# Kernel tuning notes

Measured on AMD Instinct MI355X. Metric: run time of the kernel, lower is better.

## Reference

```python
import jax, jax.numpy as jnp
import numpy as np

EPS = 1.0  # Shapelet eps
STRIDE = 1


def _shapelet(x, w, pcm):
    """x: (b,c,t), w: (n,c,l), pcm: (c,m). Returns ((b, n*c) probs, (b, n*c) dists)."""
    n, c, l = w.shape
    t = x.shape[-1]
    m = (t - l) // STRIDE + 1
    # unfold: gather overlapping windows -> (b, c, m, l)
    idx = jnp.arange(m)[:, None] * STRIDE + jnp.arange(l)[None, :]
    win = x[:, :, idx]                                   # (b, c, m, l)
    xw = jnp.transpose(win, (0, 2, 1, 3))[:, :, None]    # (b, m, 1, c, l)
    d = jnp.mean(jnp.abs(xw - w), axis=-1)               # (b, m, n, c)
    d = d * pcm.T[None, :, None, :]                      # penalty (1, m, 1, c)
    p = jnp.exp(-jnp.square(EPS * d))                    # (b, m, n, c)
    hard = jax.nn.one_hot(jnp.argmax(p, axis=1), m, axis=1, dtype=p.dtype)  # (b,m,n,c)
    soft = jax.nn.softmax(p, axis=1)
    onehot_max = hard + soft - jax.lax.stop_gradient(soft)  # straight-through
    max_p = jnp.sum(onehot_max * p, axis=1)              # (b, n, c)
    d_min = jnp.min(d, axis=1)                           # (b, n, c)
    b = x.shape[0]
    return max_p.reshape(b, -1), d_min.reshape(b, -1)


def _diversity(w):
    """w: (n,c,l) -> scalar. torch PairwiseDistance(p=2, eps=1e-6) adds eps to diff."""
    sh = jnp.transpose(w, (1, 0, 2))                     # (c, n, l)
    diff = sh[:, None, :, :] - sh[:, :, None, :] + 1e-6
    dist = jnp.sqrt(jnp.sum(jnp.square(diff), axis=-1))  # (c, n, n)
    nsh = sh.shape[1]
    mask = 1.0 - jnp.eye(nsh, dtype=w.dtype)
    return jnp.mean(jnp.exp(-dist) * mask[None])


def setup_inputs() -> dict:
    key = jax.random.key(0)
    ks = jax.random.split(key, 6)
    b, c, t, ncls = 32, 8, 512, 10
    sls = [52, 103, 154, 256]
    ms = [t - l + 1 for l in sls]
    inp = {"x": jax.random.normal(ks[0], (b, c, t), dtype=jnp.float32)}
    for i, (l, m) in enumerate(zip(sls, ms)):
        inp[f"w{i}"] = jax.random.normal(ks[1 + i], (5, c, l), dtype=jnp.float32)
        inp[f"pcm{i}"] = jnp.ones((c, m), dtype=jnp.float32)
    inp["W_out"] = jax.random.normal(ks[5], (ncls, 160), dtype=jnp.float32) * 0.05
    return inp


def reference(x, w0, w1, w2, w3, pcm0, pcm1, pcm2, pcm3, W_out):
    # instance norm over time (torch std is unbiased, ddof=1)
    mu = jnp.mean(x, axis=-1, keepdims=True)
    sd = jnp.std(x, axis=-1, keepdims=True, ddof=1)
    xn = (x - mu) / (sd + 1e-8)

    ws = (w0, w1, w2, w3)
    pcms = (pcm0, pcm1, pcm2, pcm3)
    probs, dists = [], []
    for w, pcm in zip(ws, pcms):
        p, d = _shapelet(xn, w, pcm)
        probs.append(p)
        dists.append(d)
    shapelet_probs = jnp.concatenate(probs, axis=-1)   # (b, 160)
    shapelet_dists = jnp.concatenate(dists, axis=-1)   # (b, 160)

    # dropout is identity in eval mode
    out = shapelet_probs @ W_out.T                     # (b, num_classes)

    loss_reg = jnp.mean(jnp.abs(W_out))
    loss_div = sum(_diversity(w) for w in ws)
    loss = (0.1 * loss_reg + 0.1 * loss_div).reshape(1)
    return out, shapelet_dists, shapelet_probs, loss
```

## Files before the change

### kernel.cpp

```cpp
#include <hip/hip_runtime.h>
#include <math.h>

#define B 32
#define C 8
#define T 512
#define NSH 5
#define NCLS 10
#define NFEAT 160

#define OUT_OFF    0
#define DIST_OFF   (B * NCLS)
#define PROB_OFF   (DIST_OFF + B * NFEAT)
#define LOSS_OFF   (PROB_OFF + B * NFEAT)


template<int L, int M, int GOFF>
__device__ __forceinline__ void shapelet_task(
    const float* __restrict__ x,
    const float* __restrict__ wrow,
    const float* __restrict__ pmrow,
    float* __restrict__ out, int bc, int n)
{
    const int lane = threadIdx.x & 63;
    const int b = bc >> 3, c = bc & 7;
    const float* xrow = x + bc * T;

    const float4 u0 = *(const float4*)(xrow + lane * 4);
    const float4 u1 = *(const float4*)(xrow + 256 + lane * 4);
    float s = u0.x + u0.y + u0.z + u0.w + u1.x + u1.y + u1.z + u1.w;
    #pragma unroll
    for (int off = 32; off; off >>= 1) s += __shfl_down(s, off);
    const float mu = __shfl(s, 0) * (1.0f / T);
    float sq = (u0.x-mu)*(u0.x-mu) + (u0.y-mu)*(u0.y-mu) + (u0.z-mu)*(u0.z-mu) + (u0.w-mu)*(u0.w-mu)
             + (u1.x-mu)*(u1.x-mu) + (u1.y-mu)*(u1.y-mu) + (u1.z-mu)*(u1.z-mu) + (u1.w-mu)*(u1.w-mu);
    #pragma unroll
    for (int off = 32; off; off >>= 1) sq += __shfl_down(sq, off);
    const float var = __shfl(sq, 0) * (1.0f / (T - 1));
    const float ns = 1.0f / (sqrtf(var) + 1e-8f);
    const float nb = -mu * ns;

    const int sbase = lane * 8;
    const int sb = (sbase < M) ? sbase : 0;

    float4 a  = *(const float4*)(xrow + sb);
    float4 bb = *(const float4*)(xrow + sb + 4);
    float4 cc = *(const float4*)(xrow + sb + 8);
    a.x = fmaf(a.x, ns, nb);  a.y = fmaf(a.y, ns, nb);  a.z = fmaf(a.z, ns, nb);  a.w = fmaf(a.w, ns, nb);
    bb.x = fmaf(bb.x, ns, nb); bb.y = fmaf(bb.y, ns, nb); bb.z = fmaf(bb.z, ns, nb); bb.w = fmaf(bb.w, ns, nb);
    cc.x = fmaf(cc.x, ns, nb); cc.y = fmaf(cc.y, ns, nb); cc.z = fmaf(cc.z, ns, nb); cc.w = fmaf(cc.w, ns, nb);

    float acc[8] = {0,0,0,0,0,0,0,0};
    constexpr int LC = L & ~3;

    #pragma unroll 4
    for (int j = 0; j + 4 <= L; j += 4) {
        const float wa = wrow[j], wb = wrow[j+1], wc = wrow[j+2], wd = wrow[j+3];
        acc[0]+=fabsf(a.x-wa); acc[1]+=fabsf(a.y-wa); acc[2]+=fabsf(a.z-wa); acc[3]+=fabsf(a.w-wa);
        acc[4]+=fabsf(bb.x-wa); acc[5]+=fabsf(bb.y-wa); acc[6]+=fabsf(bb.z-wa); acc[7]+=fabsf(bb.w-wa);
        acc[0]+=fabsf(a.y-wb); acc[1]+=fabsf(a.z-wb); acc[2]+=fabsf(a.w-wb); acc[3]+=fabsf(bb.x-wb);
        acc[4]+=fabsf(bb.y-wb); acc[5]+=fabsf(bb.z-wb); acc[6]+=fabsf(bb.w-wb); acc[7]+=fabsf(cc.x-wb);
        acc[0]+=fabsf(a.z-wc); acc[1]+=fabsf(a.w-wc); acc[2]+=fabsf(bb.x-wc); acc[3]+=fabsf(bb.y-wc);
        acc[4]+=fabsf(bb.z-wc); acc[5]+=fabsf(bb.w-wc); acc[6]+=fabsf(cc.x-wc); acc[7]+=fabsf(cc.y-wc);
        acc[0]+=fabsf(a.w-wd); acc[1]+=fabsf(bb.x-wd); acc[2]+=fabsf(bb.y-wd); acc[3]+=fabsf(bb.z-wd);
        acc[4]+=fabsf(bb.w-wd); acc[5]+=fabsf(cc.x-wd); acc[6]+=fabsf(cc.y-wd); acc[7]+=fabsf(cc.z-wd);
        a = bb; bb = cc;
        int nidx = sb + j + 12;
        nidx = (nidx > T - 4) ? (T - 4) : nidx;
        cc = *(const float4*)(xrow + nidx);
        cc.x = fmaf(cc.x, ns, nb); cc.y = fmaf(cc.y, ns, nb);
        cc.z = fmaf(cc.z, ns, nb); cc.w = fmaf(cc.w, ns, nb);
    }

    if constexpr ((L & 3) != 0) {
        const float rr[12] = {a.x,a.y,a.z,a.w, bb.x,bb.y,bb.z,bb.w, cc.x,cc.y,cc.z,cc.w};
        #pragma unroll
        for (int jt = 0; jt < (L & 3); ++jt) {
            const float wj = wrow[LC + jt];
            #pragma unroll
            for (int k = 0; k < 8; ++k) acc[k] += fabsf(rr[jt + k] - wj);
        }
    }

    constexpr float invL = 1.0f / (float)L;
    float mind = INFINITY, mind2 = INFINITY;
    #pragma unroll
    for (int k = 0; k < 8; ++k) {
        const int m = sbase + k;
        if (m < M) {
            const float d = acc[k] * invL * pmrow[m];
            mind  = fminf(mind, d);
            mind2 = fminf(mind2, d * d);
        }
    }
    #pragma unroll
    for (int off = 32; off; off >>= 1) {
        mind  = fminf(mind,  __shfl_down(mind,  off));
        mind2 = fminf(mind2, __shfl_down(mind2, off));
    }
    if (lane == 0) {
        const int col = GOFF + n * C + c;
        out[DIST_OFF + b * NFEAT + col] = mind;
        out[PROB_OFF + b * NFEAT + col] = expf(-mind2);
    }
}

__global__ __launch_bounds__(256) void shapelet_kernel(
    const float* __restrict__ x,
    const float* __restrict__ w0, const float* __restrict__ w1,
    const float* __restrict__ w2, const float* __restrict__ w3,
    const float* __restrict__ p0, const float* __restrict__ p1,
    const float* __restrict__ p2, const float* __restrict__ p3,
    const float* __restrict__ Wout,
    float* __restrict__ out, float* __restrict__ wsf)
{
    const int blk = blockIdx.x;
    const int wv  = __builtin_amdgcn_readfirstlane(threadIdx.x >> 6);

    if (blk < 1280) {
        const int bc = blk / 5;
        const int gn = (blk - bc * 5) * 4 + wv;
        const int g  = gn / 5;
        const int n  = gn - g * 5;
        const int c  = bc & 7;
        switch (g) {
            case 0: shapelet_task< 52, 461,   0>(x, w0 + (n*C+c)*52,  p0 + c*461, out, bc, n); break;
            case 1: shapelet_task<103, 410,  40>(x, w1 + (n*C+c)*103, p1 + c*410, out, bc, n); break;
            case 2: shapelet_task<154, 359,  80>(x, w2 + (n*C+c)*154, p2 + c*359, out, bc, n); break;
            default:shapelet_task<256, 257, 120>(x, w3 + (n*C+c)*256, p3 + c*257, out, bc, n); break;
        }
    } else if (blk < 1440) {
        const int task = (blk - 1280) * 4 + wv;
        const int lane = threadIdx.x & 63;
        const int g  = task / 160;
        const int r  = task - g * 160;
        const int c  = r / 20;
        const int pr = r - c * 20;
        const int i  = pr >> 2;
        const int j0 = pr & 3;
        const int j  = j0 + (j0 >= i ? 1 : 0);
        const float* wptrs[4] = { w0, w1, w2, w3 };
        const int    Ls[4]    = { 52, 103, 154, 256 };
        const int L = Ls[g];
        const float* wi = wptrs[g] + (i * C + c) * L;
        const float* wj = wptrs[g] + (j * C + c) * L;
        float ss = 0.0f;
        for (int t2 = lane; t2 < L; t2 += 64) {
            const float df = wj[t2] - wi[t2] + 1e-6f;
            ss += df * df;
        }
        #pragma unroll
        for (int off = 32; off; off >>= 1) ss += __shfl_down(ss, off);
        if (lane == 0) wsf[task] = expf(-sqrtf(ss));
    } else {
        const int lane = threadIdx.x & 63;
        float rg = 0.0f;
        #pragma unroll
        for (int k2 = 0; k2 < 7; ++k2) {
            const int e = lane + k2 * 64;
            if (e < 400) rg += fabsf(Wout[wv * 400 + e]);
        }
        #pragma unroll
        for (int off = 32; off; off >>= 1) rg += __shfl_down(rg, off);
        if (lane == 0) wsf[640 + wv] = rg;
    }
}

__global__ __launch_bounds__(64) void head_kernel(
    const float* __restrict__ Wout,
    const float* __restrict__ wsf,
    float* __restrict__ out)
{
    const int blk  = blockIdx.x;
    const int lane = threadIdx.x;
    if (blk < B * NCLS) {
        const int b = blk / NCLS, k = blk - b * NCLS;
        const float* pr = out + PROB_OFF + b * NFEAT;
        const float* wr = Wout + k * NFEAT;
        float acc = 0.0f;
        #pragma unroll
        for (int r = 0; r < 3; ++r) {
            const int f = lane + r * 64;
            if (f < NFEAT) acc += pr[f] * wr[f];
        }
        #pragma unroll
        for (int off = 32; off; off >>= 1) acc += __shfl_down(acc, off);
        if (lane == 0) out[OUT_OFF + blk] = acc;
    } else {
        float dv = 0.0f, rg = 0.0f;
        #pragma unroll
        for (int r = 0; r < 10; ++r) {
            const int i = lane + r * 64;
            if (i < 640) dv += wsf[i];
        }
        if (lane < 4) rg = wsf[640 + lane];
        #pragma unroll
        for (int off = 32; off; off >>= 1) {
            dv += __shfl_down(dv, off);
            rg += __shfl_down(rg, off);
        }
        if (lane == 0)
            out[LOSS_OFF] = 0.1f * (rg * (1.0f / 1600.0f)) + 0.1f * (dv * (1.0f / 200.0f));
    }
}

extern "C" void kernel_launch(void* const* d_in, const int* in_sizes, int n_in,
                              void* d_out, int out_size, void* d_ws, size_t ws_size,
                              hipStream_t stream) {
    const float* x    = (const float*)d_in[0];
    const float* w0   = (const float*)d_in[1];
    const float* pcm0 = (const float*)d_in[2];
    const float* w1   = (const float*)d_in[3];
    const float* pcm1 = (const float*)d_in[4];
    const float* w2   = (const float*)d_in[5];
    const float* pcm2 = (const float*)d_in[6];
    const float* w3   = (const float*)d_in[7];
    const float* pcm3 = (const float*)d_in[8];
    const float* Wout = (const float*)d_in[9];
    float* out = (float*)d_out;
    float* wsf = (float*)d_ws;

    shapelet_kernel<<<1441, 256, 0, stream>>>(
        x, w0, w1, w2, w3, pcm0, pcm1, pcm2, pcm3, Wout, out, wsf);
    head_kernel<<<B * NCLS + 1, 64, 0, stream>>>(Wout, wsf, out);
}
```

Measured before the change: 111.4 us.

## Precompute normalization stats, schedule long shapelets first, tune windows per lane

A new prep kernel computes each row's instance-norm scale and bias, plus the diversity and L1 terms, and stores them in workspace. This removes the mean/variance wave reduction that every shapelet wave used to repeat. The shapelet kernel now issues the longest-shapelet groups first and gives the two long groups 6 windows per lane instead of 8. That spreads their work over more lanes and shortens the critical path. The inner loop becomes a 16-entry register ring buffer with double-buffered prefetch loads, at the cost of one extra kernel launch and a dependency through workspace.

```diff
diff --git a/kernel.cpp b/kernel.cpp
--- a/kernel.cpp
+++ b/kernel.cpp
@@ -13,124 +13,40 @@
 #define PROB_OFF   (DIST_OFF + B * NFEAT)
 #define LOSS_OFF   (PROB_OFF + B * NFEAT)
 
-
-template<int L, int M, int GOFF>
-__device__ __forceinline__ void shapelet_task(
-    const float* __restrict__ x,
-    const float* __restrict__ wrow,
-    const float* __restrict__ pmrow,
-    float* __restrict__ out, int bc, int n)
-{
-    const int lane = threadIdx.x & 63;
-    const int b = bc >> 3, c = bc & 7;
-    const float* xrow = x + bc * T;
-
-    const float4 u0 = *(const float4*)(xrow + lane * 4);
-    const float4 u1 = *(const float4*)(xrow + 256 + lane * 4);
-    float s = u0.x + u0.y + u0.z + u0.w + u1.x + u1.y + u1.z + u1.w;
-    #pragma unroll
-    for (int off = 32; off; off >>= 1) s += __shfl_down(s, off);
-    const float mu = __shfl(s, 0) * (1.0f / T);
-    float sq = (u0.x-mu)*(u0.x-mu) + (u0.y-mu)*(u0.y-mu) + (u0.z-mu)*(u0.z-mu) + (u0.w-mu)*(u0.w-mu)
-             + (u1.x-mu)*(u1.x-mu) + (u1.y-mu)*(u1.y-mu) + (u1.z-mu)*(u1.z-mu) + (u1.w-mu)*(u1.w-mu);
-    #pragma unroll
-    for (int off = 32; off; off >>= 1) sq += __shfl_down(sq, off);
-    const float var = __shfl(sq, 0) * (1.0f / (T - 1));
-    const float ns = 1.0f / (sqrtf(var) + 1e-8f);
-    const float nb = -mu * ns;
-
-    const int sbase = lane * 8;
-    const int sb = (sbase < M) ? sbase : 0;
-
-    float4 a  = *(const float4*)(xrow + sb);
-    float4 bb = *(const float4*)(xrow + sb + 4);
-    float4 cc = *(const float4*)(xrow + sb + 8);
-    a.x = fmaf(a.x, ns, nb);  a.y = fmaf(a.y, ns, nb);  a.z = fmaf(a.z, ns, nb);  a.w = fmaf(a.w, ns, nb);
-    bb.x = fmaf(bb.x, ns, nb); bb.y = fmaf(bb.y, ns, nb); bb.z = fmaf(bb.z, ns, nb); bb.w = fmaf(bb.w, ns, nb);
-    cc.x = fmaf(cc.x, ns, nb); cc.y = fmaf(cc.y, ns, nb); cc.z = fmaf(cc.z, ns, nb); cc.w = fmaf(cc.w, ns, nb);
-
-    float acc[8] = {0,0,0,0,0,0,0,0};
-    constexpr int LC = L & ~3;
-
-    #pragma unroll 4
-    for (int j = 0; j + 4 <= L; j += 4) {
-        const float wa = wrow[j], wb = wrow[j+1], wc = wrow[j+2], wd = wrow[j+3];
-        acc[0]+=fabsf(a.x-wa); acc[1]+=fabsf(a.y-wa); acc[2]+=fabsf(a.z-wa); acc[3]+=fabsf(a.w-wa);
-        acc[4]+=fabsf(bb.x-wa); acc[5]+=fabsf(bb.y-wa); acc[6]+=fabsf(bb.z-wa); acc[7]+=fabsf(bb.w-wa);
-        acc[0]+=fabsf(a.y-wb); acc[1]+=fabsf(a.z-wb); acc[2]+=fabsf(a.w-wb); acc[3]+=fabsf(bb.x-wb);
-        acc[4]+=fabsf(bb.y-wb); acc[5]+=fabsf(bb.z-wb); acc[6]+=fabsf(bb.w-wb); acc[7]+=fabsf(cc.x-wb);
-        acc[0]+=fabsf(a.z-wc); acc[1]+=fabsf(a.w-wc); acc[2]+=fabsf(bb.x-wc); acc[3]+=fabsf(bb.y-wc);
-        acc[4]+=fabsf(bb.z-wc); acc[5]+=fabsf(bb.w-wc); acc[6]+=fabsf(cc.x-wc); acc[7]+=fabsf(cc.y-wc);
-        acc[0]+=fabsf(a.w-wd); acc[1]+=fabsf(bb.x-wd); acc[2]+=fabsf(bb.y-wd); acc[3]+=fabsf(bb.z-wd);
-        acc[4]+=fabsf(bb.w-wd); acc[5]+=fabsf(cc.x-wd); acc[6]+=fabsf(cc.y-wd); acc[7]+=fabsf(cc.z-wd);
-        a = bb; bb = cc;
-        int nidx = sb + j + 12;
-        nidx = (nidx > T - 4) ? (T - 4) : nidx;
-        cc = *(const float4*)(xrow + nidx);
-        cc.x = fmaf(cc.x, ns, nb); cc.y = fmaf(cc.y, ns, nb);
-        cc.z = fmaf(cc.z, ns, nb); cc.w = fmaf(cc.w, ns, nb);
-    }
-
-    if constexpr ((L & 3) != 0) {
-        const float rr[12] = {a.x,a.y,a.z,a.w, bb.x,bb.y,bb.z,bb.w, cc.x,cc.y,cc.z,cc.w};
-        #pragma unroll
-        for (int jt = 0; jt < (L & 3); ++jt) {
-            const float wj = wrow[LC + jt];
-            #pragma unroll
-            for (int k = 0; k < 8; ++k) acc[k] += fabsf(rr[jt + k] - wj);
-        }
-    }
-
-    constexpr float invL = 1.0f / (float)L;
-    float mind = INFINITY, mind2 = INFINITY;
-    #pragma unroll
-    for (int k = 0; k < 8; ++k) {
-        const int m = sbase + k;
-        if (m < M) {
-            const float d = acc[k] * invL * pmrow[m];
-            mind  = fminf(mind, d);
-            mind2 = fminf(mind2, d * d);
-        }
-    }
-    #pragma unroll
-    for (int off = 32; off; off >>= 1) {
-        mind  = fminf(mind,  __shfl_down(mind,  off));
-        mind2 = fminf(mind2, __shfl_down(mind2, off));
-    }
-    if (lane == 0) {
-        const int col = GOFF + n * C + c;
-        out[DIST_OFF + b * NFEAT + col] = mind;
-        out[PROB_OFF + b * NFEAT + col] = expf(-mind2);
-    }
-}
-
-__global__ __launch_bounds__(256) void shapelet_kernel(
+#define MUINV_OFF 648
+
+__global__ __launch_bounds__(256) void prep_kernel(
     const float* __restrict__ x,
     const float* __restrict__ w0, const float* __restrict__ w1,
     const float* __restrict__ w2, const float* __restrict__ w3,
-    const float* __restrict__ p0, const float* __restrict__ p1,
-    const float* __restrict__ p2, const float* __restrict__ p3,
     const float* __restrict__ Wout,
-    float* __restrict__ out, float* __restrict__ wsf)
-{
-    const int blk = blockIdx.x;
-    const int wv  = __builtin_amdgcn_readfirstlane(threadIdx.x >> 6);
-
-    if (blk < 1280) {
-        const int bc = blk / 5;
-        const int gn = (blk - bc * 5) * 4 + wv;
-        const int g  = gn / 5;
-        const int n  = gn - g * 5;
-        const int c  = bc & 7;
-        switch (g) {
-            case 0: shapelet_task< 52, 461,   0>(x, w0 + (n*C+c)*52,  p0 + c*461, out, bc, n); break;
-            case 1: shapelet_task<103, 410,  40>(x, w1 + (n*C+c)*103, p1 + c*410, out, bc, n); break;
-            case 2: shapelet_task<154, 359,  80>(x, w2 + (n*C+c)*154, p2 + c*359, out, bc, n); break;
-            default:shapelet_task<256, 257, 120>(x, w3 + (n*C+c)*256, p3 + c*257, out, bc, n); break;
-        }
-    } else if (blk < 1440) {
-        const int task = (blk - 1280) * 4 + wv;
-        const int lane = threadIdx.x & 63;
+    float* __restrict__ wsf)
+{
+    const int blk  = blockIdx.x;
+    const int wv   = __builtin_amdgcn_readfirstlane(threadIdx.x >> 6);
+    const int lane = threadIdx.x & 63;
+
+    if (blk < 64) {
+        const int bc = blk * 4 + wv;
+        const float* xr = x + bc * T;
+        const float4 u0 = *(const float4*)(xr + lane * 4);
+        const float4 u1 = *(const float4*)(xr + 256 + lane * 4);
+        float s = u0.x + u0.y + u0.z + u0.w + u1.x + u1.y + u1.z + u1.w;
+        #pragma unroll
+        for (int off = 32; off; off >>= 1) s += __shfl_down(s, off);
+        const float mu = __shfl(s, 0) * (1.0f / T);
+        float sq = (u0.x-mu)*(u0.x-mu) + (u0.y-mu)*(u0.y-mu) + (u0.z-mu)*(u0.z-mu) + (u0.w-mu)*(u0.w-mu)
+                 + (u1.x-mu)*(u1.x-mu) + (u1.y-mu)*(u1.y-mu) + (u1.z-mu)*(u1.z-mu) + (u1.w-mu)*(u1.w-mu);
+        #pragma unroll
+        for (int off = 32; off; off >>= 1) sq += __shfl_down(sq, off);
+        if (lane == 0) {
+            const float var = sq * (1.0f / (T - 1));
+            const float ns  = 1.0f / (sqrtf(var) + 1e-8f);
+            wsf[MUINV_OFF + 2*bc]     = ns;
+            wsf[MUINV_OFF + 2*bc + 1] = -mu * ns;
+        }
+    } else if (blk < 224) {
+        const int task = (blk - 64) * 4 + wv;
         const int g  = task / 160;
         const int r  = task - g * 160;
         const int c  = r / 20;
@@ -152,7 +68,6 @@
         for (int off = 32; off; off >>= 1) ss += __shfl_down(ss, off);
         if (lane == 0) wsf[task] = expf(-sqrtf(ss));
     } else {
-        const int lane = threadIdx.x & 63;
         float rg = 0.0f;
         #pragma unroll
         for (int k2 = 0; k2 < 7; ++k2) {
@@ -162,6 +77,154 @@
         #pragma unroll
         for (int off = 32; off; off >>= 1) rg += __shfl_down(rg, off);
         if (lane == 0) wsf[640 + wv] = rg;
+    }
+}
+
+template<int L, int M, int GOFF, int MPL, int CW>
+__device__ __forceinline__ void shapelet_task(
+    const float* __restrict__ xrow,
+    const float* __restrict__ wrow,
+    const float* __restrict__ pmrow,
+    const float* __restrict__ minv2,
+    float* __restrict__ out, int b, int c, int n)
+{
+    const int lane  = threadIdx.x & 63;
+    const int sbase = lane * MPL;
+    const int sb = (sbase < M) ? sbase : 0;
+
+    const float ns = minv2[0];
+    const float nb = minv2[1];
+
+    float U[16];
+    float acc[MPL];
+    #pragma unroll
+    for (int k = 0; k < MPL; ++k) acc[k] = 0.0f;
+
+    auto LOADCHUNK = [&](int addr) -> float4 {
+        int a = addr; if (a > T - 4) a = T - 4;
+        if constexpr (CW == 12) {
+            return *(const float4*)(xrow + a);
+        } else {
+            const float2 lo = *(const float2*)(xrow + a);
+            const float2 hi = *(const float2*)(xrow + a + 2);
+            return float4{lo.x, lo.y, hi.x, hi.y};
+        }
+    };
+
+    if constexpr (CW == 12) {
+        #pragma unroll
+        for (int q = 0; q < 3; ++q) {
+            const float4 v = *(const float4*)(xrow + sb + q * 4);
+            U[q*4+0] = fmaf(v.x, ns, nb); U[q*4+1] = fmaf(v.y, ns, nb);
+            U[q*4+2] = fmaf(v.z, ns, nb); U[q*4+3] = fmaf(v.w, ns, nb);
+        }
+    } else {
+        #pragma unroll
+        for (int q = 0; q < 5; ++q) {
+            const float2 v = *(const float2*)(xrow + sb + q * 2);
+            U[q*2+0] = fmaf(v.x, ns, nb); U[q*2+1] = fmaf(v.y, ns, nb);
+        }
+    }
+    float4 pv0 = LOADCHUNK(sb + CW);
+    float4 pv1 = LOADCHUNK(sb + CW + 4);
+
+    int j = 0;
+
+#define PHASE(BB, PV)                                                      \
+    {                                                                      \
+        U[(BB + CW + 0) & 15] = fmaf(PV.x, ns, nb);                        \
+        U[(BB + CW + 1) & 15] = fmaf(PV.y, ns, nb);                        \
+        U[(BB + CW + 2) & 15] = fmaf(PV.z, ns, nb);                        \
+        U[(BB + CW + 3) & 15] = fmaf(PV.w, ns, nb);                        \
+        PV = LOADCHUNK(sb + j + CW + 8);                                   \
+        _Pragma("unroll")                                                  \
+        for (int jj = 0; jj < 4; ++jj) {                                   \
+            const float wj = wrow[j + jj];                                 \
+            _Pragma("unroll")                                              \
+            for (int k = 0; k < MPL; ++k)                                  \
+                acc[k] += fabsf(U[(BB + jj + k) & 15] - wj);               \
+        }                                                                  \
+        j += 4;                                                            \
+    }
+
+    constexpr int NP    = L / 4;
+    constexpr int NLOOP = NP / 4;
+    constexpr int NTAIL = NP % 4;
+    for (int it = 0; it < NLOOP; ++it) {
+        PHASE(0,  pv0)
+        PHASE(4,  pv1)
+        PHASE(8,  pv0)
+        PHASE(12, pv1)
+    }
+    if constexpr (NTAIL >= 1) PHASE(0, pv0)
+    if constexpr (NTAIL >= 2) PHASE(4, pv1)
+    if constexpr (NTAIL >= 3) PHASE(8, pv0)
+#undef PHASE
+
+    if constexpr ((L & 3) != 0) {
+        constexpr int TB = (4 * NP) & 15;
+        #pragma unroll
+        for (int jt = 0; jt < (L & 3); ++jt) {
+            const float wj = wrow[4 * NP + jt];
+            #pragma unroll
+            for (int k = 0; k < MPL; ++k)
+                acc[k] += fabsf(U[(TB + jt + k) & 15] - wj);
+        }
+    }
+
+    constexpr float invL = 1.0f / (float)L;
+    float mind = INFINITY, mind2 = INFINITY;
+    #pragma unroll
+    for (int k = 0; k < MPL; ++k) {
+        const int m = sbase + k;
+        if (m < M) {
+            const float d = acc[k] * invL * pmrow[m];
+            mind  = fminf(mind, d);
+            mind2 = fminf(mind2, d * d);
+        }
+    }
+    #pragma unroll
+    for (int off = 32; off; off >>= 1) {
+        mind  = fminf(mind,  __shfl_down(mind,  off));
+        mind2 = fminf(mind2, __shfl_down(mind2, off));
+    }
+    if (lane == 0) {
+        const int col = GOFF + n * C + c;
+        out[DIST_OFF + b * NFEAT + col] = mind;
+        out[PROB_OFF + b * NFEAT + col] = expf(-mind2);
+    }
+}
+
+__global__ __launch_bounds__(256) void shapelet_kernel(
+    const float* __restrict__ x,
+    const float* __restrict__ w0, const float* __restrict__ w1,
+    const float* __restrict__ w2, const float* __restrict__ w3,
+    const float* __restrict__ p0, const float* __restrict__ p1,
+    const float* __restrict__ p2, const float* __restrict__ p3,
+    float* __restrict__ out, const float* __restrict__ wsf)
+{
+    const int blk = blockIdx.x;
+    const int wv  = __builtin_amdgcn_readfirstlane(threadIdx.x >> 6);
+
+    int gsel, base;
+    if      (blk < 320) { gsel = 3; base = 0;   }
+    else if (blk < 640) { gsel = 2; base = 320; }
+    else if (blk < 960) { gsel = 1; base = 640; }
+    else                { gsel = 0; base = 960; }
+
+    const int lt = (blk - base) * 4 + wv;
+    const int bc = lt / 5;
+    const int n  = lt - bc * 5;
+    const int c  = bc & 7;
+    const int b  = bc >> 3;
+    const float* xr = x + bc * T;
+    const float* mi = wsf + MUINV_OFF + 2 * bc;
+
+    switch (gsel) {
+        case 3:  shapelet_task<256, 257, 120, 6, 10>(xr, w3 + (n*C+c)*256, p3 + c*257, mi, out, b, c, n); break;
+        case 2:  shapelet_task<154, 359,  80, 6, 10>(xr, w2 + (n*C+c)*154, p2 + c*359, mi, out, b, c, n); break;
+        case 1:  shapelet_task<103, 410,  40, 8, 12>(xr, w1 + (n*C+c)*103, p1 + c*410, mi, out, b, c, n); break;
+        default: shapelet_task< 52, 461,   0, 8, 12>(xr, w0 + (n*C+c)*52,  p0 + c*461, mi, out, b, c, n); break;
     }
 }
 
@@ -219,7 +282,8 @@
     float* out = (float*)d_out;
     float* wsf = (float*)d_ws;
 
-    shapelet_kernel<<<1441, 256, 0, stream>>>(
-        x, w0, w1, w2, w3, pcm0, pcm1, pcm2, pcm3, Wout, out, wsf);
+    prep_kernel<<<225, 256, 0, stream>>>(x, w0, w1, w2, w3, Wout, wsf);
+    shapelet_kernel<<<1280, 256, 0, stream>>>(
+        x, w0, w1, w2, w3, pcm0, pcm1, pcm2, pcm3, out, wsf);
     head_kernel<<<B * NCLS + 1, 64, 0, stream>>>(Wout, wsf, out);
 }
```

New measurement: 107.1 us. 3.8% less time.

## Split shapelet pipeline into prep, window-parallel distance, and reduce kernels

Applied to the files above, without the earlier changes.

The normalised input is now precomputed once into workspace by a prep kernel instead of being recomputed in every shapelet wave. Each wave now handles 64 window positions (one per lane) for all five shapelets of a channel, reusing each x load across five weight rows. It writes per-segment partial minima that a new reduce kernel combines. This trades fewer redundant normalisation reductions and more parallel waves against two extra kernel launches, workspace round-trips, and scalar strided loads of x and w. The old device-side shapelet_task helper remains but is unused.

```diff
diff --git a/kernel.cpp b/kernel.cpp
--- a/kernel.cpp
+++ b/kernel.cpp
@@ -13,124 +13,42 @@
 #define PROB_OFF   (DIST_OFF + B * NFEAT)
 #define LOSS_OFF   (PROB_OFF + B * NFEAT)
 
-
-template<int L, int M, int GOFF>
-__device__ __forceinline__ void shapelet_task(
-    const float* __restrict__ x,
-    const float* __restrict__ wrow,
-    const float* __restrict__ pmrow,
-    float* __restrict__ out, int bc, int n)
-{
-    const int lane = threadIdx.x & 63;
-    const int b = bc >> 3, c = bc & 7;
-    const float* xrow = x + bc * T;
-
-    const float4 u0 = *(const float4*)(xrow + lane * 4);
-    const float4 u1 = *(const float4*)(xrow + 256 + lane * 4);
-    float s = u0.x + u0.y + u0.z + u0.w + u1.x + u1.y + u1.z + u1.w;
-    #pragma unroll
-    for (int off = 32; off; off >>= 1) s += __shfl_down(s, off);
-    const float mu = __shfl(s, 0) * (1.0f / T);
-    float sq = (u0.x-mu)*(u0.x-mu) + (u0.y-mu)*(u0.y-mu) + (u0.z-mu)*(u0.z-mu) + (u0.w-mu)*(u0.w-mu)
-             + (u1.x-mu)*(u1.x-mu) + (u1.y-mu)*(u1.y-mu) + (u1.z-mu)*(u1.z-mu) + (u1.w-mu)*(u1.w-mu);
-    #pragma unroll
-    for (int off = 32; off; off >>= 1) sq += __shfl_down(sq, off);
-    const float var = __shfl(sq, 0) * (1.0f / (T - 1));
-    const float ns = 1.0f / (sqrtf(var) + 1e-8f);
-    const float nb = -mu * ns;
-
-    const int sbase = lane * 8;
-    const int sb = (sbase < M) ? sbase : 0;
-
-    float4 a  = *(const float4*)(xrow + sb);
-    float4 bb = *(const float4*)(xrow + sb + 4);
-    float4 cc = *(const float4*)(xrow + sb + 8);
-    a.x = fmaf(a.x, ns, nb);  a.y = fmaf(a.y, ns, nb);  a.z = fmaf(a.z, ns, nb);  a.w = fmaf(a.w, ns, nb);
-    bb.x = fmaf(bb.x, ns, nb); bb.y = fmaf(bb.y, ns, nb); bb.z = fmaf(bb.z, ns, nb); bb.w = fmaf(bb.w, ns, nb);
-    cc.x = fmaf(cc.x, ns, nb); cc.y = fmaf(cc.y, ns, nb); cc.z = fmaf(cc.z, ns, nb); cc.w = fmaf(cc.w, ns, nb);
-
-    float acc[8] = {0,0,0,0,0,0,0,0};
-    constexpr int LC = L & ~3;
-
-    #pragma unroll 4
-    for (int j = 0; j + 4 <= L; j += 4) {
-        const float wa = wrow[j], wb = wrow[j+1], wc = wrow[j+2], wd = wrow[j+3];
-        acc[0]+=fabsf(a.x-wa); acc[1]+=fabsf(a.y-wa); acc[2]+=fabsf(a.z-wa); acc[3]+=fabsf(a.w-wa);
-        acc[4]+=fabsf(bb.x-wa); acc[5]+=fabsf(bb.y-wa); acc[6]+=fabsf(bb.z-wa); acc[7]+=fabsf(bb.w-wa);
-        acc[0]+=fabsf(a.y-wb); acc[1]+=fabsf(a.z-wb); acc[2]+=fabsf(a.w-wb); acc[3]+=fabsf(bb.x-wb);
-        acc[4]+=fabsf(bb.y-wb); acc[5]+=fabsf(bb.z-wb); acc[6]+=fabsf(bb.w-wb); acc[7]+=fabsf(cc.x-wb);
-        acc[0]+=fabsf(a.z-wc); acc[1]+=fabsf(a.w-wc); acc[2]+=fabsf(bb.x-wc); acc[3]+=fabsf(bb.y-wc);
-        acc[4]+=fabsf(bb.z-wc); acc[5]+=fabsf(bb.w-wc); acc[6]+=fabsf(cc.x-wc); acc[7]+=fabsf(cc.y-wc);
-        acc[0]+=fabsf(a.w-wd); acc[1]+=fabsf(bb.x-wd); acc[2]+=fabsf(bb.y-wd); acc[3]+=fabsf(bb.z-wd);
-        acc[4]+=fabsf(bb.w-wd); acc[5]+=fabsf(cc.x-wd); acc[6]+=fabsf(cc.y-wd); acc[7]+=fabsf(cc.z-wd);
-        a = bb; bb = cc;
-        int nidx = sb + j + 12;
-        nidx = (nidx > T - 4) ? (T - 4) : nidx;
-        cc = *(const float4*)(xrow + nidx);
-        cc.x = fmaf(cc.x, ns, nb); cc.y = fmaf(cc.y, ns, nb);
-        cc.z = fmaf(cc.z, ns, nb); cc.w = fmaf(cc.w, ns, nb);
-    }
-
-    if constexpr ((L & 3) != 0) {
-        const float rr[12] = {a.x,a.y,a.z,a.w, bb.x,bb.y,bb.z,bb.w, cc.x,cc.y,cc.z,cc.w};
-        #pragma unroll
-        for (int jt = 0; jt < (L & 3); ++jt) {
-            const float wj = wrow[LC + jt];
-            #pragma unroll
-            for (int k = 0; k < 8; ++k) acc[k] += fabsf(rr[jt + k] - wj);
-        }
-    }
-
-    constexpr float invL = 1.0f / (float)L;
-    float mind = INFINITY, mind2 = INFINITY;
-    #pragma unroll
-    for (int k = 0; k < 8; ++k) {
-        const int m = sbase + k;
-        if (m < M) {
-            const float d = acc[k] * invL * pmrow[m];
-            mind  = fminf(mind, d);
-            mind2 = fminf(mind2, d * d);
-        }
-    }
-    #pragma unroll
-    for (int off = 32; off; off >>= 1) {
-        mind  = fminf(mind,  __shfl_down(mind,  off));
-        mind2 = fminf(mind2, __shfl_down(mind2, off));
-    }
-    if (lane == 0) {
-        const int col = GOFF + n * C + c;
-        out[DIST_OFF + b * NFEAT + col] = mind;
-        out[PROB_OFF + b * NFEAT + col] = expf(-mind2);
-    }
-}
-
-__global__ __launch_bounds__(256) void shapelet_kernel(
+#define XN_OFF 1024
+
+__global__ __launch_bounds__(256) void prep_kernel(
     const float* __restrict__ x,
     const float* __restrict__ w0, const float* __restrict__ w1,
     const float* __restrict__ w2, const float* __restrict__ w3,
-    const float* __restrict__ p0, const float* __restrict__ p1,
-    const float* __restrict__ p2, const float* __restrict__ p3,
     const float* __restrict__ Wout,
-    float* __restrict__ out, float* __restrict__ wsf)
-{
-    const int blk = blockIdx.x;
-    const int wv  = __builtin_amdgcn_readfirstlane(threadIdx.x >> 6);
-
-    if (blk < 1280) {
-        const int bc = blk / 5;
-        const int gn = (blk - bc * 5) * 4 + wv;
-        const int g  = gn / 5;
-        const int n  = gn - g * 5;
-        const int c  = bc & 7;
-        switch (g) {
-            case 0: shapelet_task< 52, 461,   0>(x, w0 + (n*C+c)*52,  p0 + c*461, out, bc, n); break;
-            case 1: shapelet_task<103, 410,  40>(x, w1 + (n*C+c)*103, p1 + c*410, out, bc, n); break;
-            case 2: shapelet_task<154, 359,  80>(x, w2 + (n*C+c)*154, p2 + c*359, out, bc, n); break;
-            default:shapelet_task<256, 257, 120>(x, w3 + (n*C+c)*256, p3 + c*257, out, bc, n); break;
-        }
-    } else if (blk < 1440) {
-        const int task = (blk - 1280) * 4 + wv;
-        const int lane = threadIdx.x & 63;
+    float* __restrict__ wsf)
+{
+    const int blk  = blockIdx.x;
+    const int wv   = __builtin_amdgcn_readfirstlane(threadIdx.x >> 6);
+    const int lane = threadIdx.x & 63;
+
+    if (blk < 64) {
+        const int bc = blk * 4 + wv;
+        const float* xr = x + bc * T;
+        const float4 u0 = *(const float4*)(xr + lane * 4);
+        const float4 u1 = *(const float4*)(xr + 256 + lane * 4);
+        float s = u0.x + u0.y + u0.z + u0.w + u1.x + u1.y + u1.z + u1.w;
+        #pragma unroll
+        for (int off = 32; off; off >>= 1) s += __shfl_down(s, off);
+        const float mu = __shfl(s, 0) * (1.0f / T);
+        float sq = (u0.x-mu)*(u0.x-mu) + (u0.y-mu)*(u0.y-mu) + (u0.z-mu)*(u0.z-mu) + (u0.w-mu)*(u0.w-mu)
+                 + (u1.x-mu)*(u1.x-mu) + (u1.y-mu)*(u1.y-mu) + (u1.z-mu)*(u1.z-mu) + (u1.w-mu)*(u1.w-mu);
+        #pragma unroll
+        for (int off = 32; off; off >>= 1) sq += __shfl_down(sq, off);
+        const float var = __shfl(sq, 0) * (1.0f / (T - 1));
+        const float ns  = 1.0f / (sqrtf(var) + 1e-8f);
+        const float nbv = -mu * ns;
+        float* xo = wsf + XN_OFF + bc * T;
+        const float4 o0 = { fmaf(u0.x,ns,nbv), fmaf(u0.y,ns,nbv), fmaf(u0.z,ns,nbv), fmaf(u0.w,ns,nbv) };
+        const float4 o1 = { fmaf(u1.x,ns,nbv), fmaf(u1.y,ns,nbv), fmaf(u1.z,ns,nbv), fmaf(u1.w,ns,nbv) };
+        *(float4*)(xo + lane * 4)       = o0;
+        *(float4*)(xo + 256 + lane * 4) = o1;
+    } else if (blk < 224) {
+        const int task = (blk - 64) * 4 + wv;
         const int g  = task / 160;
         const int r  = task - g * 160;
         const int c  = r / 20;
@@ -152,7 +70,6 @@
         for (int off = 32; off; off >>= 1) ss += __shfl_down(ss, off);
         if (lane == 0) wsf[task] = expf(-sqrtf(ss));
     } else {
-        const int lane = threadIdx.x & 63;
         float rg = 0.0f;
         #pragma unroll
         for (int k2 = 0; k2 < 7; ++k2) {
@@ -162,6 +79,245 @@
         #pragma unroll
         for (int off = 32; off; off >>= 1) rg += __shfl_down(rg, off);
         if (lane == 0) wsf[640 + wv] = rg;
+    }
+}
+
+template<int L, int M, int S, int GOFF>
+__device__ __forceinline__ void shapelet_task(
+    const float* __restrict__ xn,
+    const float* __restrict__ wg,
+    const float* __restrict__ pmg,
+    float* __restrict__ out, int r)
+{
+    constexpr int CL = C * L;
+    const int lane = threadIdx.x & 63;
+    const int bc = r / S;
+    const int ms = r - bc * S;
+    const int b  = bc >> 3, c = bc & 7;
+    const int m  = ms * 64 + lane;
+    const bool act = (m < M);
+    const int mm = act ? m : 0;
+    const float* xr = xn + bc * T + mm;
+    const float* wr = wg + c * L;
+
+    float a0 = 0, a1 = 0, a2 = 0, a3 = 0, a4 = 0;
+
+    float xf[8];
+    #pragma unroll
+    for (int q = 0; q < 8; ++q) xf[q] = xr[q];
+
+    constexpr int NB  = L / 8;
+    constexpr int REM = L % 8;
+    int j = 0;
+    for (int it = 0; it < NB; ++it) {
+        float nxf[8];
+        #pragma unroll
+        for (int q = 0; q < 8; ++q) {
+            int o = j + 8 + q;
+            o = (o < L) ? o : (L - 1);
+            nxf[q] = xr[o];
+        }
+        #pragma unroll
+        for (int jj = 0; jj < 8; ++jj) {
+            const float xv = xf[jj];
+            const int jo = j + jj;
+            a0 += fabsf(xv - wr[jo]);
+            a1 += fabsf(xv - wr[CL + jo]);
+            a2 += fabsf(xv - wr[2 * CL + jo]);
+            a3 += fabsf(xv - wr[3 * CL + jo]);
+            a4 += fabsf(xv - wr[4 * CL + jo]);
+        }
+        #pragma unroll
+        for (int q = 0; q < 8; ++q) xf[q] = nxf[q];
+        j += 8;
+    }
+    if constexpr (REM > 0) {
+        #pragma unroll
+        for (int jj = 0; jj < REM; ++jj) {
+            const float xv = xf[jj];
+            const int jo = NB * 8 + jj;
+            a0 += fabsf(xv - wr[jo]);
+            a1 += fabsf(xv - wr[CL + jo]);
+            a2 += fabsf(xv - wr[2 * CL + jo]);
+            a3 += fabsf(xv - wr[3 * CL + jo]);
+            a4 += fabsf(xv - wr[4 * CL + jo]);
+        }
+    }
+
+    const float pmv = pmg[c * M + mm];
+    constexpr float invL = 1.0f / (float)L;
+    const float scale = invL * pmv;
+
+    float dv[5], d2[5];
+    dv[0] = act ? a0 * scale : INFINITY;
+    dv[1] = act ? a1 * scale : INFINITY;
+    dv[2] = act ? a2 * scale : INFINITY;
+    dv[3] = act ? a3 * scale : INFINITY;
+    dv[4] = act ? a4 * scale : INFINITY;
+    #pragma unroll
+    for (int n = 0; n < 5; ++n) d2[n] = dv[n] * dv[n];
+
+    #pragma unroll
+    for (int off = 32; off; off >>= 1) {
+        #pragma unroll
+        for (int n = 0; n < 5; ++n) {
+            dv[n] = fminf(dv[n], __shfl_down(dv[n], off));
+            d2[n] = fminf(d2[n], __shfl_down(d2[n], off));
+        }
+    }
+    if (lane == 0) {
+        #pragma unroll
+        for (int n = 0; n < 5; ++n) {
+            const int col = GOFF + n * C + c;
+            out[DIST_OFF + b * NFEAT + col] = dv[n];
+            out[PROB_OFF + b * NFEAT + col] = expf(-d2[n]);
+        }
+    }
+}
+
+#define PART_OFF 200000
+
+template<int L, int M, int S, int GOFF>
+__device__ __forceinline__ void shapelet_task_p(
+    const float* __restrict__ xn,
+    const float* __restrict__ wg,
+    const float* __restrict__ pmg,
+    float* __restrict__ wsf, int r, int pbase)
+{
+    constexpr int CL = C * L;
+    const int lane = threadIdx.x & 63;
+    const int bc = r / S;
+    const int ms = r - bc * S;
+    const int c  = bc & 7;
+    const int m  = ms * 64 + lane;
+    const bool act = (m < M);
+    const int mm = act ? m : 0;
+    const float* xr = xn + bc * T + mm;
+    const float* wr = wg + c * L;
+
+    float a0 = 0, a1 = 0, a2 = 0, a3 = 0, a4 = 0;
+    float xf[8];
+    #pragma unroll
+    for (int q = 0; q < 8; ++q) xf[q] = xr[q];
+
+    constexpr int NB  = L / 8;
+    constexpr int REM = L % 8;
+    int j = 0;
+    for (int it = 0; it < NB; ++it) {
+        float nxf[8];
+        #pragma unroll
+        for (int q = 0; q < 8; ++q) {
+            int o = j + 8 + q;
+            o = (o < L) ? o : (L - 1);
+            nxf[q] = xr[o];
+        }
+        #pragma unroll
+        for (int jj = 0; jj < 8; ++jj) {
+            const float xv = xf[jj];
+            const int jo = j + jj;
+            a0 += fabsf(xv - wr[jo]);
+            a1 += fabsf(xv - wr[CL + jo]);
+            a2 += fabsf(xv - wr[2 * CL + jo]);
+            a3 += fabsf(xv - wr[3 * CL + jo]);
+            a4 += fabsf(xv - wr[4 * CL + jo]);
+        }
+        #pragma unroll
+        for (int q = 0; q < 8; ++q) xf[q] = nxf[q];
+        j += 8;
+    }
+    if constexpr (REM > 0) {
+        #pragma unroll
+        for (int jj = 0; jj < REM; ++jj) {
+            const float xv = xf[jj];
+            const int jo = NB * 8 + jj;
+            a0 += fabsf(xv - wr[jo]);
+            a1 += fabsf(xv - wr[CL + jo]);
+            a2 += fabsf(xv - wr[2 * CL + jo]);
+            a3 += fabsf(xv - wr[3 * CL + jo]);
+            a4 += fabsf(xv - wr[4 * CL + jo]);
+        }
+    }
+
+    const float pmv = pmg[c * M + mm];
+    constexpr float invL = 1.0f / (float)L;
+    const float scale = invL * pmv;
+
+    float dv[5];
+    dv[0] = act ? a0 * scale : INFINITY;
+    dv[1] = act ? a1 * scale : INFINITY;
+    dv[2] = act ? a2 * scale : INFINITY;
+    dv[3] = act ? a3 * scale : INFINITY;
+    dv[4] = act ? a4 * scale : INFINITY;
+    float d2[5];
+    #pragma unroll
+    for (int n = 0; n < 5; ++n) d2[n] = act ? dv[n] * dv[n] : INFINITY;
+
+    #pragma unroll
+    for (int off = 32; off; off >>= 1) {
+        #pragma unroll
+        for (int n = 0; n < 5; ++n) {
+            dv[n] = fminf(dv[n], __shfl_down(dv[n], off));
+            d2[n] = fminf(d2[n], __shfl_down(d2[n], off));
+        }
+    }
+    if (lane == 0) {
+        #pragma unroll
+        for (int n = 0; n < 5; ++n) {
+            float* p = wsf + pbase + ((bc * 5 + n) * S + ms) * 2;
+            p[0] = dv[n];
+            p[1] = d2[n];
+        }
+    }
+}
+
+__global__ __launch_bounds__(256, 7) void shapelet_kernel(
+    const float* __restrict__ w0, const float* __restrict__ w1,
+    const float* __restrict__ w2, const float* __restrict__ w3,
+    const float* __restrict__ p0, const float* __restrict__ p1,
+    const float* __restrict__ p2, const float* __restrict__ p3,
+    float* __restrict__ wsf)
+{
+    const int wv = __builtin_amdgcn_readfirstlane(threadIdx.x >> 6);
+    const int wt = blockIdx.x * 4 + wv;
+    const float* xn = wsf + XN_OFF;
+
+    if (wt < 1280)
+        shapelet_task_p<256, 257, 5, 120>(xn, w3, p3, wsf, wt,          PART_OFF);
+    else if (wt < 2816)
+        shapelet_task_p<154, 359, 6,  80>(xn, w2, p2, wsf, wt - 1280,   PART_OFF + 12800);
+    else if (wt < 4608)
+        shapelet_task_p<103, 410, 7,  40>(xn, w1, p1, wsf, wt - 2816,   PART_OFF + 28160);
+    else
+        shapelet_task_p< 52, 461, 8,   0>(xn, w0, p0, wsf, wt - 4608,   PART_OFF + 46080);
+}
+
+__global__ __launch_bounds__(256) void reduce_kernel(
+    const float* __restrict__ wsf, float* __restrict__ out)
+{
+    const int wv   = __builtin_amdgcn_readfirstlane(threadIdx.x >> 6);
+    const int lane = threadIdx.x & 63;
+    const int t    = blockIdx.x * 4 + wv;
+    const int bc = t >> 2, g = t & 3;
+    const int b = bc >> 3, c = bc & 7;
+
+    int S, pbase, goff;
+    switch (g) {
+        case 3:  S = 5; pbase = PART_OFF;          goff = 120; break;
+        case 2:  S = 6; pbase = PART_OFF + 12800;  goff = 80;  break;
+        case 1:  S = 7; pbase = PART_OFF + 28160;  goff = 40;  break;
+        default: S = 8; pbase = PART_OFF + 46080;  goff = 0;   break;
+    }
+    const int tot = 5 * S * 2;
+    float v = INFINITY;
+    if (lane < tot) v = wsf[pbase + (bc * 5) * S * 2 + lane];
+    if (lane < 10) {
+        const int n = lane >> 1, q = lane & 1;
+        const float* p = wsf + pbase + ((bc * 5 + n) * S) * 2 + q;
+        float mn = INFINITY;
+        for (int msi = 0; msi < S; ++msi) mn = fminf(mn, p[msi * 2]);
+        const int col = goff + n * C + c;
+        if (q == 0) out[DIST_OFF + b * NFEAT + col] = mn;
+        else        out[PROB_OFF + b * NFEAT + col] = expf(-mn);
     }
 }
 
@@ -219,7 +375,9 @@
     float* out = (float*)d_out;
     float* wsf = (float*)d_ws;
 
-    shapelet_kernel<<<1441, 256, 0, stream>>>(
-        x, w0, w1, w2, w3, pcm0, pcm1, pcm2, pcm3, Wout, out, wsf);
+    prep_kernel<<<225, 256, 0, stream>>>(x, w0, w1, w2, w3, Wout, wsf);
+    shapelet_kernel<<<1664, 256, 0, stream>>>(
+        w0, w1, w2, w3, pcm0, pcm1, pcm2, pcm3, wsf);
+    reduce_kernel<<<256, 256, 0, stream>>>(wsf, out);
     head_kernel<<<B * NCLS + 1, 64, 0, stream>>>(Wout, wsf, out);
 }
```

New measurement: 102.5 us. 8.0% less time.
